# Performance work log

Measured on AMD Instinct MI355X. Metric: run time of the kernel, lower is better.

The kernel has to match this reference:

```python
import jax, jax.numpy as jnp
import numpy as np

V, C, BLK = 32000, 512, 2048
B, T = 4, 2048
EPS = 1e-5


def _layernorm(x, g, b):
    mu = jnp.mean(x, axis=-1, keepdims=True)
    var = jnp.mean(jnp.square(x - mu), axis=-1, keepdims=True)
    return (x - mu) * jax.lax.rsqrt(var + EPS) * g + b


def setup_inputs() -> dict:
    key = jax.random.key(0)
    ks = jax.random.split(key, 16)
    s = 0.02
    return {
        "idx": jax.random.randint(ks[0], (B, T), 0, V),
        "targets": jax.random.randint(ks[1], (B, T), 0, V),
        "tok_emb": jax.random.normal(ks[2], (V, C), jnp.float32) * s,
        "pos_emb": jax.random.normal(ks[3], (BLK, C), jnp.float32) * s,
        "Wk": jax.random.normal(ks[4], (C, C), jnp.float32) * s,
        "Wq": jax.random.normal(ks[5], (C, C), jnp.float32) * s,
        "Wv": jax.random.normal(ks[6], (C, C), jnp.float32) * s,
        "W1": jax.random.normal(ks[7], (4 * C, C), jnp.float32) * s,
        "b1": jnp.zeros((4 * C,), jnp.float32),
        "W2": jax.random.normal(ks[8], (C, 4 * C), jnp.float32) * s,
        "b2": jnp.zeros((C,), jnp.float32),
        "g1": jnp.ones((C,), jnp.float32),
        "beta1": jnp.zeros((C,), jnp.float32),
        "g2": jnp.ones((C,), jnp.float32),
        "beta2": jnp.zeros((C,), jnp.float32),
        "Wlm": jax.random.normal(ks[9], (V, C), jnp.float32) * s,
        "blm": jnp.zeros((V,), jnp.float32),
    }


def reference(idx, targets, tok_emb, pos_emb, Wk, Wq, Wv, W1, b1, W2, b2,
              g1, beta1, g2, beta2, Wlm, blm):
    # embeddings
    x = tok_emb[idx] + pos_emb[:T]  # [B,T,C]
    # single-head causal self-attention (dropout = identity, eval mode)
    h = _layernorm(x, g1, beta1)
    q = jnp.einsum('btc,dc->btd', h, Wq)
    k = jnp.einsum('btc,dc->btd', h, Wk)
    v = jnp.einsum('btc,dc->btd', h, Wv)
    wei = jnp.einsum('btd,bsd->bts', q, k) * (C ** -0.5)  # [B,T,T]
    mask = jnp.tril(jnp.ones((T, T), bool))
    wei = jnp.where(mask, wei, -jnp.inf)
    wei = jax.nn.softmax(wei, axis=-1)
    x = x + jnp.einsum('bts,bsd->btd', wei, v)
    # FFN
    h2 = _layernorm(x, g2, beta2)
    ff = jax.nn.relu(jnp.einsum('btc,fc->btf', h2, W1) + b1)
    x = x + jnp.einsum('btf,cf->btc', ff, W2) + b2
    # lm head + cross-entropy
    logits = (jnp.einsum('btc,vc->btv', x, Wlm) + blm).reshape(B * T, V)
    logp = jax.nn.log_softmax(logits, axis=-1)
    loss = -jnp.mean(jnp.take_along_axis(logp, targets.reshape(-1, 1), axis=1))
    return logits, loss
```

## Files before the change

kernel.cpp:

```cpp
#include <hip/hip_runtime.h>

typedef __bf16 bf16;
typedef __bf16 bf16x8 __attribute__((ext_vector_type(8)));
typedef float  f32x4  __attribute__((ext_vector_type(4)));

#define NB 4
#define NT 2048
#define NC 512
#define NV 32000
#define NROWS (NB*NT)
#define NCHUNK 500
#define LNEPS 1e-5f
#define SMEM_B 131072

static __device__ __forceinline__ void load_lds16(const bf16* g, char* l) {
  __builtin_amdgcn_global_load_lds(
      (const __attribute__((address_space(1))) void*)g,
      (__attribute__((address_space(3))) void*)l, 16, 0, 0);
}

static __device__ __forceinline__ void bar() {
  asm volatile("" ::: "memory");
  __builtin_amdgcn_s_barrier();
  asm volatile("" ::: "memory");
}

__global__ __launch_bounds__(256)
void cvt_kernel(const float* __restrict__ in, bf16* __restrict__ out, int n8) {
  long i = (long)blockIdx.x * 256 + threadIdx.x;
  long stride = (long)gridDim.x * 256;
  for (; i < n8; i += stride) {
    const float* p = in + i * 8;
    f32x4 a = *(const f32x4*)p;
    f32x4 b = *(const f32x4*)(p + 4);
    bf16x8 o;
    o[0]=(bf16)a.x; o[1]=(bf16)a.y; o[2]=(bf16)a.z; o[3]=(bf16)a.w;
    o[4]=(bf16)b.x; o[5]=(bf16)b.y; o[6]=(bf16)b.z; o[7]=(bf16)b.w;
    *(bf16x8*)(out + i*8) = o;
  }
}

__global__ __launch_bounds__(64)
void embed_ln_kernel(const int* __restrict__ idx, const float* __restrict__ tok,
                     const float* __restrict__ pos, const float* __restrict__ gw,
                     const float* __restrict__ bw,
                     float* __restrict__ x0, bf16* __restrict__ h1) {
  int row = blockIdx.x;
  int t = row & (NT-1);
  int id = idx[row];
  int lane = threadIdx.x;
  const float* tr = tok + (long)id*NC + lane*8;
  const float* pr = pos + (long)t*NC + lane*8;
  f32x4 a0 = *(const f32x4*)tr, a1 = *(const f32x4*)(tr+4);
  f32x4 p0 = *(const f32x4*)pr, p1 = *(const f32x4*)(pr+4);
  f32x4 r0 = a0 + p0, r1 = a1 + p1;
  float* o = x0 + (long)row*NC + lane*8;
  *(f32x4*)o = r0; *(f32x4*)(o+4) = r1;
  float v[8] = {r0.x,r0.y,r0.z,r0.w,r1.x,r1.y,r1.z,r1.w};
  float s = 0.f;
  #pragma unroll
  for (int j=0;j<8;++j) s += v[j];
  #pragma unroll
  for (int m=32;m>=1;m>>=1) s += __shfl_xor(s, m);
  float mu = s * (1.f/NC);
  float sq = 0.f;
  #pragma unroll
  for (int j=0;j<8;++j) { v[j] -= mu; sq += v[j]*v[j]; }
  #pragma unroll
  for (int m=32;m>=1;m>>=1) sq += __shfl_xor(sq, m);
  float rs = rsqrtf(sq * (1.f/NC) + LNEPS);
  const float* gp = gw + lane*8;
  const float* bp = bw + lane*8;
  f32x4 g0 = *(const f32x4*)gp, g1 = *(const f32x4*)(gp+4);
  f32x4 b0 = *(const f32x4*)bp, b1 = *(const f32x4*)(bp+4);
  float gg[8] = {g0.x,g0.y,g0.z,g0.w,g1.x,g1.y,g1.z,g1.w};
  float bb[8] = {b0.x,b0.y,b0.z,b0.w,b1.x,b1.y,b1.z,b1.w};
  bf16x8 oo;
  #pragma unroll
  for (int j=0;j<8;++j) oo[j] = (bf16)(v[j]*rs*gg[j] + bb[j]);
  *(bf16x8*)(h1 + (long)row*NC + lane*8) = oo;
}

__global__ __launch_bounds__(256)
void transpose_kernel(const bf16* __restrict__ v, long ldv, bf16* __restrict__ vt) {
  __shared__ bf16 tile[64][66];
  int b = blockIdx.z;
  int t0 = blockIdx.x*64, c0 = blockIdx.y*64;
  int tid = threadIdx.x;
  int r = tid >> 2, ch = (tid & 3) * 16;
  const bf16* src = v + ((long)b*NT + t0 + r)*ldv + c0 + ch;
  #pragma unroll
  for (int i=0;i<16;++i) tile[r][ch+i] = src[i];
  __syncthreads();
  bf16x8 o0, o1;
  #pragma unroll
  for (int i=0;i<8;++i) o0[i] = tile[ch+i][r];
  #pragma unroll
  for (int i=0;i<8;++i) o1[i] = tile[ch+8+i][r];
  bf16* dst = vt + ((long)b*NC + c0 + r)*NT + t0 + ch;
  *(bf16x8*)dst = o0;
  *(bf16x8*)(dst+8) = o1;
}

__global__ __launch_bounds__(256)
void softmax_kernel(float* __restrict__ S) {
  const int row = blockIdx.x;
  const int t = row & (NT-1);
  const int tid = threadIdx.x;
  float* sr = S + (long)row*NT;
  bf16* pr = (bf16*)S + (long)row*(2*NT);
  const float scale = 0.044194173824159216f;
  f32x4 v0 = *(const f32x4*)(sr + tid*8);
  f32x4 v1 = *(const f32x4*)(sr + tid*8 + 4);
  float v[8] = {v0.x,v0.y,v0.z,v0.w,v1.x,v1.y,v1.z,v1.w};
  int cb = tid*8;
  float mx = -1e30f;
  #pragma unroll
  for (int j=0;j<8;++j) {
    v[j] = (cb + j <= t) ? v[j]*scale : -1e30f;
    mx = fmaxf(mx, v[j]);
  }
  __shared__ float redm[4];
  #pragma unroll
  for (int m=32;m>=1;m>>=1) mx = fmaxf(mx, __shfl_xor(mx, m));
  if ((tid & 63) == 0) redm[tid>>6] = mx;
  __syncthreads();
  mx = fmaxf(fmaxf(redm[0],redm[1]), fmaxf(redm[2],redm[3]));
  float e[8]; float s = 0.f;
  #pragma unroll
  for (int j=0;j<8;++j) { e[j] = (cb + j <= t) ? __expf(v[j]-mx) : 0.f; s += e[j]; }
  __shared__ float reds[4];
  #pragma unroll
  for (int m=32;m>=1;m>>=1) s += __shfl_xor(s, m);
  if ((tid & 63) == 0) reds[tid>>6] = s;
  __syncthreads();
  s = reds[0]+reds[1]+reds[2]+reds[3];
  float inv = 1.f/s;
  bf16x8 o;
  #pragma unroll
  for (int j=0;j<8;++j) o[j] = (bf16)(e[j]*inv);
  *(bf16x8*)(pr + cb) = o;
}

enum { EPI_F32=0, EPI_BF16=1, EPI_BIAS_RELU_BF16=2, EPI_BIAS_RES_BF16=3, EPI_RES_F32=4 };

template<int EPI, bool CAUSAL=false, bool SWAP=false, bool KCHUNK=false>
__global__ __launch_bounds__(512,2)
void gemm256(const bf16* __restrict__ A, const bf16* __restrict__ B, int nkt,
             long lda, long ldb, long sAb, long sBb,
             float* __restrict__ outf, bf16* __restrict__ outb, long ldo, long sOb,
             const float* __restrict__ bias,
             const float* __restrict__ res, long ldr, long sRb) {
  extern __shared__ char smem[];
  int bn, bm;
  if constexpr (SWAP) { bm = blockIdx.x; bn = blockIdx.y; }
  else               { bn = blockIdx.x; bm = blockIdx.y; }
  const int bz = blockIdx.z;
  if constexpr (CAUSAL) { if (bn > bm) return; }
  int nkt_eff = nkt;
  int bzAB = bz;
  long kOff = 0;
  if constexpr (KCHUNK) {
    int c = bz >> 2; bzAB = bz & 3;
    int lim = (bm+1)*4 - c*8;
    if (lim <= 0) return;
    if (lim < nkt_eff) nkt_eff = lim;
    kOff = (long)c*512;
  }

  const int tid = threadIdx.x;
  const int wid = tid >> 6, lane = tid & 63;
  const int wr = wid >> 2, wc = wid & 3;
  const int l15 = lane & 15, g = lane >> 4;

  const bf16* Ab = A + (long)bzAB*sAb + kOff + (long)bm*256*lda;
  const bf16* Bb = B + (long)bzAB*sBb + kOff + (long)bn*256*ldb;

  const int colsw = 8 * ((tid & 7) ^ ((tid >> 3) & 7));
  const bf16* A0 = Ab + (long)(tid >> 3)*lda + colsw;
  const bf16* B0 = Bb + (long)(tid >> 3)*ldb + colsw;

  auto stage = [&](int ab, int t, int h, int slot) {
    char* dst = smem + slot*65536 + ab*32768 + h*16384 + wid*1024;
    const bf16* s0 = (ab ? B0 : A0) + (long)(h*128)*(ab ? ldb : lda) + (long)t*64;
    load_lds16(s0, dst);
    load_lds16(s0 + 64*(ab ? ldb : lda), dst + 8192);
  };

  const char* sm = smem;
  auto aLoad = [&](int slot, int m, int kk) -> bf16x8 {
    int row = m*16 + l15;
    int b = row*128 + ((kk*64 + g*16) ^ ((row & 7) << 4));
    return *(const bf16x8*)(sm + slot*65536 + wr*16384 + b);
  };
  auto bLoad = [&](int slot, int n, int kk) -> bf16x8 {
    int row = (wc & 1)*64 + n*16 + l15;
    int b = row*128 + ((kk*64 + g*16) ^ ((row & 7) << 4));
    return *(const bf16x8*)(sm + slot*65536 + 32768 + (wc >> 1)*16384 + b);
  };

  f32x4 acc[8][4] = {};

  stage(0, 0, 0, 0);
  stage(0, 0, 1, 0);
  stage(1, 0, 0, 0);
  stage(1, 0, 1, 0);
  stage(0, 1, 0, 1);
  asm volatile("s_waitcnt vmcnt(2)" ::: "memory");
  bar();

  const int niter = nkt_eff >> 1;
  for (int it = 0; it < niter; ++it) {
    const int t0 = 2*it, t1 = 2*it + 1;
    const int tn0 = (t0+2 < nkt_eff) ? t0+2 : nkt_eff-1;
    const int tn1 = (t1+2 < nkt_eff) ? t1+2 : nkt_eff-1;
    bf16x8 a0[4][2], a1[4][2], b0[2][2], b1[2][2];

    #pragma unroll
    for (int m=0;m<4;++m) { a0[m][0]=aLoad(0,m,0); a0[m][1]=aLoad(0,m,1); }
    #pragma unroll
    for (int n=0;n<2;++n) { b0[n][0]=bLoad(0,n,0); b0[n][1]=bLoad(0,n,1); }
    stage(0, t1, 1, 1);
    bar();
    __builtin_amdgcn_s_setprio(1);
    #pragma unroll
    for (int m=0;m<4;++m)
      #pragma unroll
      for (int n=0;n<2;++n) {
        acc[m][n] = __builtin_amdgcn_mfma_f32_16x16x32_bf16(a0[m][0], b0[n][0], acc[m][n],0,0,0);
        acc[m][n] = __builtin_amdgcn_mfma_f32_16x16x32_bf16(a0[m][1], b0[n][1], acc[m][n],0,0,0);
      }
    __builtin_amdgcn_s_setprio(0);
    bar();
    #pragma unroll
    for (int n=0;n<2;++n) { b1[n][0]=bLoad(0,n+2,0); b1[n][1]=bLoad(0,n+2,1); }
    stage(1, t1, 0, 1);
    bar();
    __builtin_amdgcn_s_setprio(1);
    #pragma unroll
    for (int m=0;m<4;++m)
      #pragma unroll
      for (int n=0;n<2;++n) {
        acc[m][n+2] = __builtin_amdgcn_mfma_f32_16x16x32_bf16(a0[m][0], b1[n][0], acc[m][n+2],0,0,0);
        acc[m][n+2] = __builtin_amdgcn_mfma_f32_16x16x32_bf16(a0[m][1], b1[n][1], acc[m][n+2],0,0,0);
      }
    __builtin_amdgcn_s_setprio(0);
    bar();
    #pragma unroll
    for (int m=0;m<4;++m) { a1[m][0]=aLoad(0,m+4,0); a1[m][1]=aLoad(0,m+4,1); }
    stage(1, t1, 1, 1);
    bar();
    __builtin_amdgcn_s_setprio(1);
    #pragma unroll
    for (int m=0;m<4;++m)
      #pragma unroll
      for (int n=0;n<2;++n) {
        acc[m+4][n+2] = __builtin_amdgcn_mfma_f32_16x16x32_bf16(a1[m][0], b1[n][0], acc[m+4][n+2],0,0,0);
        acc[m+4][n+2] = __builtin_amdgcn_mfma_f32_16x16x32_bf16(a1[m][1], b1[n][1], acc[m+4][n+2],0,0,0);
      }
    __builtin_amdgcn_s_setprio(0);
    bar();
    stage(0, tn0, 0, 0);
    asm volatile("s_waitcnt vmcnt(2)" ::: "memory");
    bar();
    __builtin_amdgcn_s_setprio(1);
    #pragma unroll
    for (int m=0;m<4;++m)
      #pragma unroll
      for (int n=0;n<2;++n) {
        acc[m+4][n] = __builtin_amdgcn_mfma_f32_16x16x32_bf16(a1[m][0], b0[n][0], acc[m+4][n],0,0,0);
        acc[m+4][n] = __builtin_amdgcn_mfma_f32_16x16x32_bf16(a1[m][1], b0[n][1], acc[m+4][n],0,0,0);
      }
    __builtin_amdgcn_s_setprio(0);
    bar();
    #pragma unroll
    for (int m=0;m<4;++m) { a0[m][0]=aLoad(1,m,0); a0[m][1]=aLoad(1,m,1); }
    #pragma unroll
    for (int n=0;n<2;++n) { b0[n][0]=bLoad(1,n,0); b0[n][1]=bLoad(1,n,1); }
    stage(0, tn0, 1, 0);
    bar();
    __builtin_amdgcn_s_setprio(1);
    #pragma unroll
    for (int m=0;m<4;++m)
      #pragma unroll
      for (int n=0;n<2;++n) {
        acc[m][n] = __builtin_amdgcn_mfma_f32_16x16x32_bf16(a0[m][0], b0[n][0], acc[m][n],0,0,0);
        acc[m][n] = __builtin_amdgcn_mfma_f32_16x16x32_bf16(a0[m][1], b0[n][1], acc[m][n],0,0,0);
      }
    __builtin_amdgcn_s_setprio(0);
    bar();
    #pragma unroll
    for (int n=0;n<2;++n) { b1[n][0]=bLoad(1,n+2,0); b1[n][1]=bLoad(1,n+2,1); }
    stage(1, tn0, 0, 0);
    bar();
    __builtin_amdgcn_s_setprio(1);
    #pragma unroll
    for (int m=0;m<4;++m)
      #pragma unroll
      for (int n=0;n<2;++n) {
        acc[m][n+2] = __builtin_amdgcn_mfma_f32_16x16x32_bf16(a0[m][0], b1[n][0], acc[m][n+2],0,0,0);
        acc[m][n+2] = __builtin_amdgcn_mfma_f32_16x16x32_bf16(a0[m][1], b1[n][1], acc[m][n+2],0,0,0);
      }
    __builtin_amdgcn_s_setprio(0);
    bar();
    #pragma unroll
    for (int m=0;m<4;++m) { a1[m][0]=aLoad(1,m+4,0); a1[m][1]=aLoad(1,m+4,1); }
    stage(1, tn0, 1, 0);
    bar();
    __builtin_amdgcn_s_setprio(1);
    #pragma unroll
    for (int m=0;m<4;++m)
      #pragma unroll
      for (int n=0;n<2;++n) {
        acc[m+4][n+2] = __builtin_amdgcn_mfma_f32_16x16x32_bf16(a1[m][0], b1[n][0], acc[m+4][n+2],0,0,0);
        acc[m+4][n+2] = __builtin_amdgcn_mfma_f32_16x16x32_bf16(a1[m][1], b1[n][1], acc[m+4][n+2],0,0,0);
      }
    __builtin_amdgcn_s_setprio(0);
    bar();
    stage(0, tn1, 0, 1);
    asm volatile("s_waitcnt vmcnt(2)" ::: "memory");
    bar();
    __builtin_amdgcn_s_setprio(1);
    #pragma unroll
    for (int m=0;m<4;++m)
      #pragma unroll
      for (int n=0;n<2;++n) {
        acc[m+4][n] = __builtin_amdgcn_mfma_f32_16x16x32_bf16(a1[m][0], b0[n][0], acc[m+4][n],0,0,0);
        acc[m+4][n] = __builtin_amdgcn_mfma_f32_16x16x32_bf16(a1[m][1], b0[n][1], acc[m+4][n],0,0,0);
      }
    __builtin_amdgcn_s_setprio(0);
    bar();
  }

  const long rowbase = (long)bm*256 + wr*128;
  const long colbase = (long)bn*256 + wc*64;

  #pragma unroll
  for (int m=0;m<8;++m)
    #pragma unroll
    for (int n=0;n<4;++n) {
      long c = colbase + n*16 + l15;
      #pragma unroll
      for (int q_=0;q_<4;++q_) {
        long rr = rowbase + m*16 + g*4 + q_;
        float v = acc[m][n][q_];
        if constexpr (EPI == EPI_F32) {
          outf[(long)bz*sOb + rr*ldo + c] = v;
        } else if constexpr (EPI == EPI_BF16) {
          outb[(long)bz*sOb + rr*ldo + c] = (bf16)v;
        } else if constexpr (EPI == EPI_BIAS_RELU_BF16) {
          outb[rr*ldo + c] = (bf16)fmaxf(v + bias[c], 0.f);
        } else if constexpr (EPI == EPI_BIAS_RES_BF16) {
          outb[rr*ldo + c] = (bf16)(v + bias[c] + res[rr*ldr + c]);
        } else if constexpr (EPI == EPI_RES_F32) {
          outf[(long)bz*sOb + rr*ldo + c] = v + res[(long)bz*sRb + rr*ldr + c];
        }
      }
    }
}

__global__ __launch_bounds__(256,4)
void lmhead128(const bf16* __restrict__ A, const bf16* __restrict__ B,
               const float* __restrict__ bias, float* __restrict__ outf,
               float* __restrict__ pmax, float* __restrict__ psum) {
  __shared__ char sm[32768];
  const int bm = blockIdx.x, bn = blockIdx.y;
  const int tid = threadIdx.x;
  const int wid = tid >> 6, lane = tid & 63;
  const int wr = wid >> 1, wc = wid & 1;
  const int l15 = lane & 15, g = lane >> 4;

  const int p0 = tid, p1 = tid + 256;
  const int r0_ = 2*(p0>>3) + ((p0>>2)&1), c0_ = 8*((p0&3) ^ ((p0>>3)&3));
  const int r1_ = 2*(p1>>3) + ((p1>>2)&1), c1_ = 8*((p1&3) ^ ((p1>>3)&3));
  const bf16* A00 = A + ((long)bm*128 + r0_)*NC + c0_;
  const bf16* A01 = A + ((long)bm*128 + r1_)*NC + c1_;
  const bf16* B00 = B + ((long)bn*128 + r0_)*NC + c0_;
  const bf16* B01 = B + ((long)bn*128 + r1_)*NC + c1_;

  auto stage = [&](int kt, int slot) {
    char* base = sm + slot*16384 + wid*1024;
    load_lds16(A00 + kt*32, base);
    load_lds16(A01 + kt*32, base + 4096);
    load_lds16(B00 + kt*32, base + 8192);
    load_lds16(B01 + kt*32, base + 12288);
  };

  auto aLoad = [&](int slot, int m) -> bf16x8 {
    int R = wr*64 + m*16 + l15;
    return *(const bf16x8*)(sm + slot*16384 + (R>>1)*128 + (R&1)*64
                            + ((g ^ ((R>>1)&3)) << 4));
  };
  auto bLoad = [&](int slot, int n) -> bf16x8 {
    int R = wc*64 + n*16 + l15;
    return *(const bf16x8*)(sm + slot*16384 + 8192 + (R>>1)*128 + (R&1)*64
                            + ((g ^ ((R>>1)&3)) << 4));
  };

  f32x4 acc[4][4] = {};

  stage(0, 0);
  asm volatile("s_waitcnt vmcnt(0)" ::: "memory");
  bar();

  int cur = 0;
  for (int kt = 0; kt < 16; ++kt) {
    if (kt < 15) stage(kt + 1, cur ^ 1);
    bf16x8 af[4], bf_[4];
    #pragma unroll
    for (int m=0;m<4;++m) af[m] = aLoad(cur, m);
    #pragma unroll
    for (int n=0;n<4;++n) bf_[n] = bLoad(cur, n);
    __builtin_amdgcn_s_setprio(1);
    #pragma unroll
    for (int m=0;m<4;++m)
      #pragma unroll
      for (int n=0;n<4;++n)
        acc[m][n] = __builtin_amdgcn_mfma_f32_16x16x32_bf16(af[m], bf_[n], acc[m][n],0,0,0);
    __builtin_amdgcn_s_setprio(0);
    asm volatile("s_waitcnt vmcnt(0)" ::: "memory");
    bar();
    cur ^= 1;
  }

  const long rowb = (long)bm*128;
  const long colb = (long)bn*128;
  #pragma unroll
  for (int n=0;n<4;++n) {
    float bv = bias[colb + wc*64 + n*16 + l15];
    #pragma unroll
    for (int m=0;m<4;++m)
      #pragma unroll
      for (int q=0;q<4;++q) acc[m][n][q] += bv;
  }
  #pragma unroll
  for (int m=0;m<4;++m)
    #pragma unroll
    for (int q=0;q<4;++q) {
      float mx = fmaxf(fmaxf(acc[m][0][q], acc[m][1][q]),
                       fmaxf(acc[m][2][q], acc[m][3][q]));
      #pragma unroll
      for (int msk=8;msk>=1;msk>>=1) mx = fmaxf(mx, __shfl_xor(mx, msk));
      float se = 0.f;
      #pragma unroll
      for (int n=0;n<4;++n) se += __expf(acc[m][n][q] - mx);
      #pragma unroll
      for (int msk=8;msk>=1;msk>>=1) se += __shfl_xor(se, msk);
      if (l15 == 0) {
        long row = rowb + wr*64 + m*16 + g*4 + q;
        pmax[row*NCHUNK + bn*2 + wc] = mx;
        psum[row*NCHUNK + bn*2 + wc] = se;
      }
    }
  #pragma unroll
  for (int m=0;m<4;++m)
    #pragma unroll
    for (int n=0;n<4;++n) {
      long c = colb + wc*64 + n*16 + l15;
      #pragma unroll
      for (int q=0;q<4;++q) {
        long rr = rowb + wr*64 + m*16 + g*4 + q;
        __builtin_nontemporal_store(acc[m][n][q], &outf[rr*NV + c]);
      }
    }
}

__global__ __launch_bounds__(64)
void pv_combine_ln_kernel(const float* __restrict__ part, const float* __restrict__ x0,
                          const float* __restrict__ gw, const float* __restrict__ bw,
                          float* __restrict__ x1, bf16* __restrict__ h2) {
  int row = blockIdx.x;
  int b = row >> 11, t = row & (NT-1);
  int lane = threadIdx.x;
  int nC = (t >> 9) + 1;
  const float* xr = x0 + (long)row*NC + lane*8;
  f32x4 a0 = *(const f32x4*)xr, a1 = *(const f32x4*)(xr+4);
  for (int c = 0; c < nC; ++c) {
    const float* pr = part + ((long)(c*4 + b)*NT + t)*NC + lane*8;
    a0 += *(const f32x4*)pr; a1 += *(const f32x4*)(pr+4);
  }
  float* o = x1 + (long)row*NC + lane*8;
  *(f32x4*)o = a0; *(f32x4*)(o+4) = a1;
  float v[8] = {a0.x,a0.y,a0.z,a0.w,a1.x,a1.y,a1.z,a1.w};
  float s = 0.f;
  #pragma unroll
  for (int j=0;j<8;++j) s += v[j];
  #pragma unroll
  for (int m=32;m>=1;m>>=1) s += __shfl_xor(s, m);
  float mu = s * (1.f/NC);
  float sq = 0.f;
  #pragma unroll
  for (int j=0;j<8;++j) { v[j] -= mu; sq += v[j]*v[j]; }
  #pragma unroll
  for (int m=32;m>=1;m>>=1) sq += __shfl_xor(sq, m);
  float rs = rsqrtf(sq * (1.f/NC) + LNEPS);
  const float* gp = gw + lane*8;
  const float* bp = bw + lane*8;
  f32x4 g0 = *(const f32x4*)gp, g1 = *(const f32x4*)(gp+4);
  f32x4 b0 = *(const f32x4*)bp, b1 = *(const f32x4*)(bp+4);
  float gg[8] = {g0.x,g0.y,g0.z,g0.w,g1.x,g1.y,g1.z,g1.w};
  float bb[8] = {b0.x,b0.y,b0.z,b0.w,b1.x,b1.y,b1.z,b1.w};
  bf16x8 oo;
  #pragma unroll
  for (int j=0;j<8;++j) oo[j] = (bf16)(v[j]*rs*gg[j] + bb[j]);
  *(bf16x8*)(h2 + (long)row*NC + lane*8) = oo;
}

__global__ __launch_bounds__(64)
void ffn2_combine_kernel(const float* __restrict__ part, const float* __restrict__ x1,
                         const float* __restrict__ b2, bf16* __restrict__ x2) {
  int row = blockIdx.x;
  int lane = threadIdx.x;
  const float* xr = x1 + (long)row*NC + lane*8;
  f32x4 a0 = *(const f32x4*)xr, a1 = *(const f32x4*)(xr+4);
  const float* br = b2 + lane*8;
  a0 += *(const f32x4*)br; a1 += *(const f32x4*)(br+4);
  #pragma unroll
  for (int z = 0; z < 4; ++z) {
    const float* pr = part + ((long)z*NROWS + row)*NC + lane*8;
    a0 += *(const f32x4*)pr; a1 += *(const f32x4*)(pr+4);
  }
  bf16x8 o;
  o[0]=(bf16)a0.x; o[1]=(bf16)a0.y; o[2]=(bf16)a0.z; o[3]=(bf16)a0.w;
  o[4]=(bf16)a1.x; o[5]=(bf16)a1.y; o[6]=(bf16)a1.z; o[7]=(bf16)a1.w;
  *(bf16x8*)(x2 + (long)row*NC + lane*8) = o;
}

__global__ __launch_bounds__(512)
void loss1_kernel(const float* __restrict__ pmax, const float* __restrict__ psum,
                  const float* __restrict__ logits, const int* __restrict__ targets,
                  float* __restrict__ rowloss) {
  int row = blockIdx.x;
  int tid = threadIdx.x;
  int lane = tid & 63, wv = tid >> 6;
  float cm = (tid < NCHUNK) ? pmax[(long)row*NCHUNK + tid] : -1e30f;
  float cs = (tid < NCHUNK) ? psum[(long)row*NCHUNK + tid] : 0.f;
  float mx = cm;
  #pragma unroll
  for (int m=32;m>=1;m>>=1) mx = fmaxf(mx, __shfl_xor(mx, m));
  __shared__ float rm[8];
  if (lane == 0) rm[wv] = mx;
  __syncthreads();
  float M = rm[0];
  #pragma unroll
  for (int i=1;i<8;++i) M = fmaxf(M, rm[i]);
  float sc = cs * __expf(cm - M);
  #pragma unroll
  for (int m=32;m>=1;m>>=1) sc += __shfl_xor(sc, m);
  __shared__ float rs_[8];
  if (lane == 0) rs_[wv] = sc;
  __syncthreads();
  if (tid == 0) {
    float Sv = 0.f;
    #pragma unroll
    for (int i=0;i<8;++i) Sv += rs_[i];
    float lse = M + logf(Sv);
    int tgt = targets[row];
    float lg = logits[(long)row*NV + tgt];
    rowloss[row] = lse - lg;
  }
}

__global__ __launch_bounds__(256)
void loss2_kernel(const float* __restrict__ rowloss, float* __restrict__ out) {
  int tid = threadIdx.x;
  float s = 0.f;
  for (int i = tid; i < NROWS; i += 256) s += rowloss[i];
  #pragma unroll
  for (int m=32;m>=1;m>>=1) s += __shfl_xor(s, m);
  __shared__ float rs_[4];
  if ((tid & 63) == 0) rs_[tid>>6] = s;
  __syncthreads();
  if (tid == 0) out[0] = (rs_[0]+rs_[1]+rs_[2]+rs_[3]) * (1.f/NROWS);
}

extern "C" void kernel_launch(void* const* d_in, const int* in_sizes, int n_in,
                              void* d_out, int out_size, void* d_ws, size_t ws_size,
                              hipStream_t stream) {
  const int*   idx  = (const int*)d_in[0];
  const int*   tgt  = (const int*)d_in[1];
  const float* tok  = (const float*)d_in[2];
  const float* pos  = (const float*)d_in[3];
  const float* Wk   = (const float*)d_in[4];
  const float* Wq   = (const float*)d_in[5];
  const float* Wv   = (const float*)d_in[6];
  const float* W1   = (const float*)d_in[7];
  const float* b1   = (const float*)d_in[8];
  const float* W2   = (const float*)d_in[9];
  const float* b2   = (const float*)d_in[10];
  const float* g1   = (const float*)d_in[11];
  const float* be1  = (const float*)d_in[12];
  const float* g2   = (const float*)d_in[13];
  const float* be2  = (const float*)d_in[14];
  const float* Wlm  = (const float*)d_in[15];
  const float* blm  = (const float*)d_in[16];

  float* logits = (float*)d_out;
  float* loss   = logits + (long)NROWS*NV;

  char* w = (char*)d_ws;
  auto alloc = [&](size_t bytes) -> char* {
    char* p = w; w += (bytes + 255) & ~(size_t)255; return p;
  };
  bf16* wqkvb = (bf16*)alloc((size_t)3*NC*NC*2);
  bf16* w1b   = (bf16*)alloc((size_t)4*NC*NC*2);
  bf16* w2b   = (bf16*)alloc((size_t)4*NC*NC*2);
  bf16* wlmb  = (bf16*)alloc((size_t)NV*NC*2);
  float* x0   = (float*)alloc((size_t)NROWS*NC*4);
  bf16* h1b   = (bf16*)alloc((size_t)NROWS*NC*2);
  bf16* qkvb  = (bf16*)alloc((size_t)NROWS*3*NC*2);
  bf16* vtb   = (bf16*)alloc((size_t)NROWS*NC*2);
  float* Sb   = (float*)alloc((size_t)NB*NT*NT*4);
  float* pvp  = (float*)alloc((size_t)16*NT*NC*4);
  float* x1   = (float*)alloc((size_t)NROWS*NC*4);
  bf16* h2b   = (bf16*)alloc((size_t)NROWS*NC*2);
  bf16* ffb   = (bf16*)alloc((size_t)NROWS*4*NC*2);
  bf16* x2b   = (bf16*)alloc((size_t)NROWS*NC*2);
  float* pmax = (float*)alloc((size_t)NROWS*NCHUNK*4);
  float* psum = (float*)alloc((size_t)NROWS*NCHUNK*4);
  float* rowloss = (float*)alloc((size_t)NROWS*4);
  float* ff2p = Sb;

  hipFuncSetAttribute((const void*)gemm256<EPI_BF16,false,false,false>,
                      hipFuncAttributeMaxDynamicSharedMemorySize, SMEM_B);
  hipFuncSetAttribute((const void*)gemm256<EPI_F32,true,false,false>,
                      hipFuncAttributeMaxDynamicSharedMemorySize, SMEM_B);
  hipFuncSetAttribute((const void*)gemm256<EPI_F32,false,false,true>,
                      hipFuncAttributeMaxDynamicSharedMemorySize, SMEM_B);
  hipFuncSetAttribute((const void*)gemm256<EPI_F32,false,false,false>,
                      hipFuncAttributeMaxDynamicSharedMemorySize, SMEM_B);
  hipFuncSetAttribute((const void*)gemm256<EPI_BIAS_RELU_BF16,false,true,false>,
                      hipFuncAttributeMaxDynamicSharedMemorySize, SMEM_B);

  auto cvt = [&](const float* in, bf16* out, long n) {
    int n8 = (int)(n/8);
    int blocks = (n8 + 255)/256; if (blocks > 2048) blocks = 2048;
    cvt_kernel<<<blocks, 256, 0, stream>>>(in, out, n8);
  };
  cvt(Wq, wqkvb, (long)NC*NC);
  cvt(Wk, wqkvb + (long)NC*NC, (long)NC*NC);
  cvt(Wv, wqkvb + (long)2*NC*NC, (long)NC*NC);
  cvt(W1, w1b, (long)4*NC*NC);
  cvt(W2, w2b, (long)4*NC*NC);
  cvt(Wlm, wlmb, (long)NV*NC);

  embed_ln_kernel<<<NROWS, 64, 0, stream>>>(idx, tok, pos, g1, be1, x0, h1b);

  gemm256<EPI_BF16><<<dim3(6,32,1), 512, SMEM_B, stream>>>(
      h1b, wqkvb, 8, NC, NC, 0, 0, nullptr, qkvb, 3*NC, 0,
      nullptr, nullptr, 0, 0);

  transpose_kernel<<<dim3(NT/64, NC/64, NB), 256, 0, stream>>>(qkvb + 2*NC, 3*NC, vtb);

  gemm256<EPI_F32,true><<<dim3(8,8,NB), 512, SMEM_B, stream>>>(
      qkvb, qkvb + NC, 8, 3*NC, 3*NC, (long)NT*3*NC, (long)NT*3*NC,
      Sb, nullptr, NT, (long)NT*NT,
      nullptr, nullptr, 0, 0);

  softmax_kernel<<<NROWS, 256, 0, stream>>>(Sb);

  gemm256<EPI_F32,false,false,true><<<dim3(2,8,16), 512, SMEM_B, stream>>>(
      (const bf16*)Sb, vtb, 8, 2*NT, NT, (long)NT*2*NT, (long)NC*NT,
      pvp, nullptr, NC, (long)NT*NC,
      nullptr, nullptr, 0, 0);

  pv_combine_ln_kernel<<<NROWS, 64, 0, stream>>>(pvp, x0, g2, be2, x1, h2b);

  gemm256<EPI_BIAS_RELU_BF16,false,true><<<dim3(32,8,1), 512, SMEM_B, stream>>>(
      h2b, w1b, 8, NC, NC, 0, 0, nullptr, ffb, 4*NC, 0,
      b1, nullptr, 0, 0);

  gemm256<EPI_F32><<<dim3(2,32,4), 512, SMEM_B, stream>>>(
      ffb, w2b, 8, 4*NC, 4*NC, 512, 512,
      ff2p, nullptr, NC, (long)NROWS*NC,
      nullptr, nullptr, 0, 0);

  ffn2_combine_kernel<<<NROWS, 64, 0, stream>>>(ff2p, x1, b2, x2b);

  lmhead128<<<dim3(64, NV/128), 256, 0, stream>>>(x2b, wlmb, blm, logits, pmax, psum);

  loss1_kernel<<<NROWS, 512, 0, stream>>>(pmax, psum, logits, tgt, rowloss);
  loss2_kernel<<<1, 256, 0, stream>>>(rowloss, loss);
}
```

Baseline: 742.5 us.

## Run LM head on the 256x256 GEMM kernel with fused softmax-partial epilogue

Replaces the dedicated 128x128-tile LM-head kernel with the larger 256x256-tile, 512-thread pipelined GEMM, adding an epilogue mode that applies the bias, writes per-64-column max/sum partials, and stages outputs through LDS so logits go out as coalesced 16-byte nontemporal stores. The larger tile is meant to raise arithmetic intensity and reduce operand reloads for the biggest GEMM, and the vector stores target the cost of the 128MB logits write. The partial index now uses bn*4+wc, which stays within NCHUNK=500 for 125 column blocks. The tradeoffs are fewer blocks (4000 instead of 16000) and a possible tail effect on a 125x32 grid.

```diff
diff --git a/kernel.cpp b/kernel.cpp
--- a/kernel.cpp
+++ b/kernel.cpp
@@ -142,7 +142,7 @@
   *(bf16x8*)(pr + cb) = o;
 }
 
-enum { EPI_F32=0, EPI_BF16=1, EPI_BIAS_RELU_BF16=2, EPI_BIAS_RES_BF16=3, EPI_RES_F32=4 };
+enum { EPI_F32=0, EPI_BF16=1, EPI_BIAS_RELU_BF16=2, EPI_BIAS_RES_BF16=3, EPI_RES_F32=4, EPI_LMHEAD=5 };
 
 template<int EPI, bool CAUSAL=false, bool SWAP=false, bool KCHUNK=false>
 __global__ __launch_bounds__(512,2)
@@ -150,7 +150,8 @@
              long lda, long ldb, long sAb, long sBb,
              float* __restrict__ outf, bf16* __restrict__ outb, long ldo, long sOb,
              const float* __restrict__ bias,
-             const float* __restrict__ res, long ldr, long sRb) {
+             const float* __restrict__ res, long ldr, long sRb,
+             float* __restrict__ pmax = nullptr, float* __restrict__ psum = nullptr) {
   extern __shared__ char smem[];
   int bn, bm;
   if constexpr (SWAP) { bm = blockIdx.x; bn = blockIdx.y; }
@@ -335,134 +336,74 @@
   const long rowbase = (long)bm*256 + wr*128;
   const long colbase = (long)bn*256 + wc*64;
 
-  #pragma unroll
-  for (int m=0;m<8;++m)
+  if constexpr (EPI == EPI_LMHEAD) {
     #pragma unroll
     for (int n=0;n<4;++n) {
-      long c = colbase + n*16 + l15;
+      float bv = bias[colbase + n*16 + l15];
+      #pragma unroll
+      for (int m=0;m<8;++m)
+        #pragma unroll
+        for (int q_=0;q_<4;++q_) acc[m][n][q_] += bv;
+    }
+    #pragma unroll
+    for (int m=0;m<8;++m)
       #pragma unroll
       for (int q_=0;q_<4;++q_) {
-        long rr = rowbase + m*16 + g*4 + q_;
-        float v = acc[m][n][q_];
-        if constexpr (EPI == EPI_F32) {
-          outf[(long)bz*sOb + rr*ldo + c] = v;
-        } else if constexpr (EPI == EPI_BF16) {
-          outb[(long)bz*sOb + rr*ldo + c] = (bf16)v;
-        } else if constexpr (EPI == EPI_BIAS_RELU_BF16) {
-          outb[rr*ldo + c] = (bf16)fmaxf(v + bias[c], 0.f);
-        } else if constexpr (EPI == EPI_BIAS_RES_BF16) {
-          outb[rr*ldo + c] = (bf16)(v + bias[c] + res[rr*ldr + c]);
-        } else if constexpr (EPI == EPI_RES_F32) {
-          outf[(long)bz*sOb + rr*ldo + c] = v + res[(long)bz*sRb + rr*ldr + c];
+        float mx = fmaxf(fmaxf(acc[m][0][q_], acc[m][1][q_]),
+                         fmaxf(acc[m][2][q_], acc[m][3][q_]));
+        #pragma unroll
+        for (int msk=8;msk>=1;msk>>=1) mx = fmaxf(mx, __shfl_xor(mx, msk));
+        float se = 0.f;
+        #pragma unroll
+        for (int n=0;n<4;++n) se += __expf(acc[m][n][q_] - mx);
+        #pragma unroll
+        for (int msk=8;msk>=1;msk>>=1) se += __shfl_xor(se, msk);
+        if (l15 == 0) {
+          long row = rowbase + m*16 + g*4 + q_;
+          pmax[row*NCHUNK + bn*4 + wc] = mx;
+          psum[row*NCHUNK + bn*4 + wc] = se;
         }
       }
+    float* lbuf = (float*)(smem + wid*4096);
+    #pragma unroll
+    for (int m=0;m<8;++m) {
+      #pragma unroll
+      for (int n=0;n<4;++n)
+        #pragma unroll
+        for (int q_=0;q_<4;++q_)
+          lbuf[(g*4+q_)*64 + n*16 + l15] = acc[m][n][q_];
+      #pragma unroll
+      for (int p=0;p<4;++p) {
+        f32x4 v = *(const f32x4*)&lbuf[(p*4+g)*64 + l15*4];
+        long row = rowbase + m*16 + p*4 + g;
+        long col = colbase + l15*4;
+        __builtin_nontemporal_store(v, (f32x4*)&outf[row*ldo + col]);
+      }
     }
-}
-
-__global__ __launch_bounds__(256,4)
-void lmhead128(const bf16* __restrict__ A, const bf16* __restrict__ B,
-               const float* __restrict__ bias, float* __restrict__ outf,
-               float* __restrict__ pmax, float* __restrict__ psum) {
-  __shared__ char sm[32768];
-  const int bm = blockIdx.x, bn = blockIdx.y;
-  const int tid = threadIdx.x;
-  const int wid = tid >> 6, lane = tid & 63;
-  const int wr = wid >> 1, wc = wid & 1;
-  const int l15 = lane & 15, g = lane >> 4;
-
-  const int p0 = tid, p1 = tid + 256;
-  const int r0_ = 2*(p0>>3) + ((p0>>2)&1), c0_ = 8*((p0&3) ^ ((p0>>3)&3));
-  const int r1_ = 2*(p1>>3) + ((p1>>2)&1), c1_ = 8*((p1&3) ^ ((p1>>3)&3));
-  const bf16* A00 = A + ((long)bm*128 + r0_)*NC + c0_;
-  const bf16* A01 = A + ((long)bm*128 + r1_)*NC + c1_;
-  const bf16* B00 = B + ((long)bn*128 + r0_)*NC + c0_;
-  const bf16* B01 = B + ((long)bn*128 + r1_)*NC + c1_;
-
-  auto stage = [&](int kt, int slot) {
-    char* base = sm + slot*16384 + wid*1024;
-    load_lds16(A00 + kt*32, base);
-    load_lds16(A01 + kt*32, base + 4096);
-    load_lds16(B00 + kt*32, base + 8192);
-    load_lds16(B01 + kt*32, base + 12288);
-  };
-
-  auto aLoad = [&](int slot, int m) -> bf16x8 {
-    int R = wr*64 + m*16 + l15;
-    return *(const bf16x8*)(sm + slot*16384 + (R>>1)*128 + (R&1)*64
-                            + ((g ^ ((R>>1)&3)) << 4));
-  };
-  auto bLoad = [&](int slot, int n) -> bf16x8 {
-    int R = wc*64 + n*16 + l15;
-    return *(const bf16x8*)(sm + slot*16384 + 8192 + (R>>1)*128 + (R&1)*64
-                            + ((g ^ ((R>>1)&3)) << 4));
-  };
-
-  f32x4 acc[4][4] = {};
-
-  stage(0, 0);
-  asm volatile("s_waitcnt vmcnt(0)" ::: "memory");
-  bar();
-
-  int cur = 0;
-  for (int kt = 0; kt < 16; ++kt) {
-    if (kt < 15) stage(kt + 1, cur ^ 1);
-    bf16x8 af[4], bf_[4];
-    #pragma unroll
-    for (int m=0;m<4;++m) af[m] = aLoad(cur, m);
-    #pragma unroll
-    for (int n=0;n<4;++n) bf_[n] = bLoad(cur, n);
-    __builtin_amdgcn_s_setprio(1);
-    #pragma unroll
-    for (int m=0;m<4;++m)
-      #pragma unroll
-      for (int n=0;n<4;++n)
-        acc[m][n] = __builtin_amdgcn_mfma_f32_16x16x32_bf16(af[m], bf_[n], acc[m][n],0,0,0);
-    __builtin_amdgcn_s_setprio(0);
-    asm volatile("s_waitcnt vmcnt(0)" ::: "memory");
-    bar();
-    cur ^= 1;
-  }
-
-  const long rowb = (long)bm*128;
-  const long colb = (long)bn*128;
-  #pragma unroll
-  for (int n=0;n<4;++n) {
-    float bv = bias[colb + wc*64 + n*16 + l15];
-    #pragma unroll
-    for (int m=0;m<4;++m)
-      #pragma unroll
-      for (int q=0;q<4;++q) acc[m][n][q] += bv;
-  }
-  #pragma unroll
-  for (int m=0;m<4;++m)
-    #pragma unroll
-    for (int q=0;q<4;++q) {
-      float mx = fmaxf(fmaxf(acc[m][0][q], acc[m][1][q]),
-                       fmaxf(acc[m][2][q], acc[m][3][q]));
-      #pragma unroll
-      for (int msk=8;msk>=1;msk>>=1) mx = fmaxf(mx, __shfl_xor(mx, msk));
-      float se = 0.f;
-      #pragma unroll
-      for (int n=0;n<4;++n) se += __expf(acc[m][n][q] - mx);
-      #pragma unroll
-      for (int msk=8;msk>=1;msk>>=1) se += __shfl_xor(se, msk);
-      if (l15 == 0) {
-        long row = rowb + wr*64 + m*16 + g*4 + q;
-        pmax[row*NCHUNK + bn*2 + wc] = mx;
-        psum[row*NCHUNK + bn*2 + wc] = se;
-      }
-    }
-  #pragma unroll
-  for (int m=0;m<4;++m)
-    #pragma unroll
-    for (int n=0;n<4;++n) {
-      long c = colb + wc*64 + n*16 + l15;
-      #pragma unroll
-      for (int q=0;q<4;++q) {
-        long rr = rowb + wr*64 + m*16 + g*4 + q;
-        __builtin_nontemporal_store(acc[m][n][q], &outf[rr*NV + c]);
-      }
-    }
+  } else {
+    #pragma unroll
+    for (int m=0;m<8;++m)
+      #pragma unroll
+      for (int n=0;n<4;++n) {
+        long c = colbase + n*16 + l15;
+        #pragma unroll
+        for (int q_=0;q_<4;++q_) {
+          long rr = rowbase + m*16 + g*4 + q_;
+          float v = acc[m][n][q_];
+          if constexpr (EPI == EPI_F32) {
+            outf[(long)bz*sOb + rr*ldo + c] = v;
+          } else if constexpr (EPI == EPI_BF16) {
+            outb[(long)bz*sOb + rr*ldo + c] = (bf16)v;
+          } else if constexpr (EPI == EPI_BIAS_RELU_BF16) {
+            outb[rr*ldo + c] = (bf16)fmaxf(v + bias[c], 0.f);
+          } else if constexpr (EPI == EPI_BIAS_RES_BF16) {
+            outb[rr*ldo + c] = (bf16)(v + bias[c] + res[rr*ldr + c]);
+          } else if constexpr (EPI == EPI_RES_F32) {
+            outf[(long)bz*sOb + rr*ldo + c] = v + res[(long)bz*sRb + rr*ldr + c];
+          }
+        }
+      }
+  }
 }
 
 __global__ __launch_bounds__(64)
@@ -631,6 +572,8 @@
                       hipFuncAttributeMaxDynamicSharedMemorySize, SMEM_B);
   hipFuncSetAttribute((const void*)gemm256<EPI_BIAS_RELU_BF16,false,true,false>,
                       hipFuncAttributeMaxDynamicSharedMemorySize, SMEM_B);
+  hipFuncSetAttribute((const void*)gemm256<EPI_LMHEAD,false,true,false>,
+                      hipFuncAttributeMaxDynamicSharedMemorySize, SMEM_B);
 
   auto cvt = [&](const float* in, bf16* out, long n) {
     int n8 = (int)(n/8);
@@ -677,7 +620,9 @@
 
   ffn2_combine_kernel<<<NROWS, 64, 0, stream>>>(ff2p, x1, b2, x2b);
 
-  lmhead128<<<dim3(64, NV/128), 256, 0, stream>>>(x2b, wlmb, blm, logits, pmax, psum);
+  gemm256<EPI_LMHEAD,false,true><<<dim3(32,125,1), 512, SMEM_B, stream>>>(
+      x2b, wlmb, 8, NC, NC, 0, 0, logits, nullptr, NV, 0,
+      blm, nullptr, 0, 0, pmax, psum);
 
   loss1_kernel<<<NROWS, 512, 0, stream>>>(pmax, psum, logits, tgt, rowloss);
   loss2_kernel<<<1, 256, 0, stream>>>(rowloss, loss);
```

Measured after the change: 792.1 us. +6.7%, slower.
